# Performance work log

Measured on AMD Instinct MI355X. Metric: run time of the kernel, lower is better.

The kernel has to match this reference:

```python
import jax, jax.numpy as jnp
import numpy as np


def _gcn_conv(x, W, b, src, dst, n_nodes):
    """PyG-style GCNConv: XW, symmetric deg^-1/2 normalization over edges
    (with self-loops already included in src/dst), scatter-add to targets, + bias."""
    xw = x @ W  # [N, F_out]
    ones = jnp.ones(src.shape[0], dtype=xw.dtype)
    deg = jax.ops.segment_sum(ones, dst, num_segments=n_nodes)  # in-degree incl. self-loops
    dinv = jnp.where(deg > 0, jax.lax.rsqrt(jnp.maximum(deg, 1.0)), 0.0)
    norm = dinv[src] * dinv[dst]                        # [E]
    msgs = xw[src] * norm[:, None]                      # [E, F_out] gather + scale
    out = jax.ops.segment_sum(msgs, dst, num_segments=n_nodes)  # scatter-add
    return out + b


def setup_inputs() -> dict:
    key = jax.random.key(0)
    k1, k2, k3, k4 = jax.random.split(key, 4)
    N, E = 100000, 1600000
    IN, HID, OUT = 128, 64, 64
    x = jax.random.normal(k1, (N, IN), dtype=jnp.float32)
    edge_index = jax.random.randint(k2, (2, E), 0, N, dtype=jnp.int64)
    W1 = jax.random.normal(k3, (IN, HID), dtype=jnp.float32) * (1.0 / np.sqrt(IN))
    b1 = jnp.zeros((HID,), dtype=jnp.float32)
    W2 = jax.random.normal(k4, (HID, OUT), dtype=jnp.float32) * (1.0 / np.sqrt(HID))
    b2 = jnp.zeros((OUT,), dtype=jnp.float32)
    return {"x": x, "edge_index": edge_index, "W1": W1, "b1": b1, "W2": W2, "b2": b2}


def reference(x, edge_index, W1, b1, W2, b2):
    n_nodes = x.shape[0]
    # add self-loops (PyG GCNConv default add_self_loops=True)
    loops = jnp.arange(n_nodes, dtype=edge_index.dtype)
    src = jnp.concatenate([edge_index[0], loops])
    dst = jnp.concatenate([edge_index[1], loops])
    h = _gcn_conv(x, W1, b1, src, dst, n_nodes)
    h = jax.nn.relu(h)
    z = _gcn_conv(h, W2, b2, src, dst, n_nodes)
    return z
```

## Files before the change

### kernel.cpp

```cpp
#include <hip/hip_runtime.h>

#define IN_F 128
#define HID_F 64
#define BKT_SHIFT 9
#define BKT_SIZE 512
#define CHUNK 4096

typedef unsigned short ushort_t;
typedef __attribute__((ext_vector_type(8))) short bf16x8;
typedef __attribute__((ext_vector_type(4))) float f32x4;

__device__ inline ushort_t f2bf(float f) {
    unsigned u = __float_as_uint(f);
    u += 0x7FFFu + ((u >> 16) & 1u);
    return (ushort_t)(u >> 16);
}
__device__ inline float bf2f(ushort_t u) {
    return __uint_as_float((unsigned)u << 16);
}


__global__ __launch_bounds__(256) void k_bcount(const int* __restrict__ dst,
        int* __restrict__ gcount, int E) {
    __shared__ int hist[256];
    int tid = threadIdx.x;
    hist[tid] = 0;
    __syncthreads();
    int e0 = blockIdx.x * CHUNK, e1 = min(e0 + CHUNK, E);
    for (int e = e0 + tid; e < e1; e += 256)
        atomicAdd(&hist[dst[e] >> BKT_SHIFT], 1);
    __syncthreads();
    if (hist[tid]) atomicAdd(&gcount[tid], hist[tid]);
}

__global__ __launch_bounds__(256) void k_bscan(const int* __restrict__ gcount,
        int* __restrict__ bbase, int* __restrict__ gcursor,
        int* __restrict__ rowptr, int N, int E) {
    __shared__ int s[256];
    int tid = threadIdx.x;
    int c = gcount[tid];
    s[tid] = c;
    __syncthreads();
    for (int off = 1; off < 256; off <<= 1) {
        int v = (tid >= off) ? s[tid - off] : 0;
        __syncthreads();
        s[tid] += v;
        __syncthreads();
    }
    int excl = s[tid] - c;
    bbase[tid] = excl;
    gcursor[tid] = excl;
    if (tid == 255) bbase[256] = s[255];
    if (tid == 0) rowptr[N] = E;
}

__global__ __launch_bounds__(256) void k_bin(const int* __restrict__ src,
        const int* __restrict__ dst, int* __restrict__ gcursor,
        unsigned* __restrict__ gbin, int E) {
    __shared__ int hist[256];
    __shared__ int cur[256];
    int tid = threadIdx.x;
    hist[tid] = 0;
    __syncthreads();
    int e0 = blockIdx.x * CHUNK, e1 = min(e0 + CHUNK, E);
    for (int e = e0 + tid; e < e1; e += 256)
        atomicAdd(&hist[dst[e] >> BKT_SHIFT], 1);
    __syncthreads();
    if (hist[tid]) cur[tid] = atomicAdd(&gcursor[tid], hist[tid]);
    __syncthreads();
    for (int e = e0 + tid; e < e1; e += 256) {
        int d = dst[e];
        int b = d >> BKT_SHIFT;
        int p = atomicAdd(&cur[b], 1);
        gbin[p] = ((unsigned)(d & (BKT_SIZE - 1)) << 23) | (unsigned)src[e];
    }
}

__global__ __launch_bounds__(256) void k_fill2(const unsigned* __restrict__ gbin,
        const int* __restrict__ bbase, int* __restrict__ rowptr,
        float* __restrict__ dinv, int* __restrict__ col, int N) {
    __shared__ int cnt[BKT_SIZE];
    __shared__ int pos[BKT_SIZE];
    __shared__ int s[256];
    int tid = threadIdx.x;
    int b = blockIdx.x;
    int e0 = bbase[b], e1 = bbase[b + 1];
    cnt[tid] = 0; cnt[tid + 256] = 0;
    __syncthreads();
    for (int e = e0 + tid; e < e1; e += 256)
        atomicAdd(&cnt[gbin[e] >> 23], 1);
    __syncthreads();
    int c0 = cnt[2 * tid], c1 = cnt[2 * tid + 1];
    int p2 = c0 + c1;
    s[tid] = p2;
    __syncthreads();
    for (int off = 1; off < 256; off <<= 1) {
        int v = (tid >= off) ? s[tid - off] : 0;
        __syncthreads();
        s[tid] += v;
        __syncthreads();
    }
    int excl = s[tid] - p2;
    pos[2 * tid] = excl;
    pos[2 * tid + 1] = excl + c0;
    __syncthreads();
    int n0 = b << BKT_SHIFT;
    #pragma unroll
    for (int i = tid; i < BKT_SIZE; i += 256) {
        int n = n0 + i;
        if (n < N) {
            rowptr[n] = e0 + pos[i];
            dinv[n] = rsqrtf((float)cnt[i] + 1.0f);
        }
    }
    __syncthreads();
    for (int e = e0 + tid; e < e1; e += 256) {
        unsigned v = gbin[e];
        int p = atomicAdd(&pos[v >> 23], 1);
        col[e0 + p] = (int)(v & 0x7FFFFFu);
    }
}

__global__ void k_pack(const float* __restrict__ W1, const float* __restrict__ W2,
                       ushort_t* __restrict__ Bp1, ushort_t* __restrict__ Bp2) {
    int tid = blockIdx.x * 256 + threadIdx.x;
    int id = (tid < 8192) ? tid : tid - 8192;
    int j = id & 7, lane = (id >> 3) & 63, t = (id >> 9) & 3, s = id >> 11;
    int k = s * 32 + ((lane >> 4) << 3) + j;
    int n = t * 16 + (lane & 15);
    if (tid < 8192)        Bp1[id] = f2bf(W1[k * 64 + n]);
    else if (tid < 12288)  Bp2[id] = f2bf(W2[k * 64 + n]);
}

template<int K, typename AT>
__global__ __launch_bounds__(256) void k_gemm_mfma(const AT* __restrict__ A,
        const ushort_t* __restrict__ Bp, const float* __restrict__ dinv,
        ushort_t* __restrict__ out, int N) {
    int wave = threadIdx.x >> 6, lane = threadIdx.x & 63;
    int m = lane & 15, q = lane >> 4;
    int row0 = blockIdx.x * 64 + wave * 16;
    int arow = row0 + m;
    int arowc = (arow < N) ? arow : (N - 1);
    f32x4 acc[4] = {};
    #pragma unroll
    for (int s = 0; s < K / 32; ++s) {
        bf16x8 af;
        if constexpr (sizeof(AT) == 4) {
            const float* ap = (const float*)A + (size_t)arowc * K + s * 32 + q * 8;
            float4 x0 = *(const float4*)ap;
            float4 x1 = *(const float4*)(ap + 4);
            af[0] = (short)f2bf(x0.x); af[1] = (short)f2bf(x0.y);
            af[2] = (short)f2bf(x0.z); af[3] = (short)f2bf(x0.w);
            af[4] = (short)f2bf(x1.x); af[5] = (short)f2bf(x1.y);
            af[6] = (short)f2bf(x1.z); af[7] = (short)f2bf(x1.w);
        } else {
            af = *(const bf16x8*)((const ushort_t*)A + (size_t)arowc * K + s * 32 + q * 8);
        }
        #pragma unroll
        for (int t = 0; t < 4; ++t) {
            bf16x8 bf = *(const bf16x8*)(Bp + (size_t)((s * 4 + t) * 64 + lane) * 8);
            acc[t] = __builtin_amdgcn_mfma_f32_16x16x32_bf16(af, bf, acc[t], 0, 0, 0);
        }
    }
    int orow0 = row0 + q * 4;
    float4 d4 = *(const float4*)(dinv + orow0);
    #pragma unroll
    for (int r = 0; r < 4; ++r) {
        int row = orow0 + r;
        if (row < N) {
            float dn = (r == 0) ? d4.x : (r == 1) ? d4.y : (r == 2) ? d4.z : d4.w;
            #pragma unroll
            for (int t = 0; t < 4; ++t)
                out[(size_t)row * 64 + t * 16 + m] = f2bf(acc[t][r] * dn);
        }
    }
}

__global__ __launch_bounds__(256) void k_aggregate(const ushort_t* __restrict__ xws,
        const int* __restrict__ rowptr, const int* __restrict__ col,
        const float* __restrict__ dinv, const float* __restrict__ bias,
        float* __restrict__ outf, ushort_t* __restrict__ outb, int N, int relu_bf16) {
    int n = (blockIdx.x * 256 + threadIdx.x) >> 4;
    int i = threadIdx.x & 15;
    if (n >= N) return;
    int beg = rowptr[n], end = rowptr[n + 1];
    float dn = dinv[n];
    const ushort_t* base = xws + i * 4;
    ushort4 sv = *(const ushort4*)(base + (size_t)n * 64);
    float ac[4][4] = {};
    ac[0][0] = bf2f(sv.x); ac[0][1] = bf2f(sv.y);
    ac[0][2] = bf2f(sv.z); ac[0][3] = bf2f(sv.w);
    int e = beg;
    for (; e + 4 <= end; e += 4) {
        int c0 = col[e + 0], c1 = col[e + 1], c2 = col[e + 2], c3 = col[e + 3];
        ushort4 v0 = *(const ushort4*)(base + (size_t)c0 * 64);
        ushort4 v1 = *(const ushort4*)(base + (size_t)c1 * 64);
        ushort4 v2 = *(const ushort4*)(base + (size_t)c2 * 64);
        ushort4 v3 = *(const ushort4*)(base + (size_t)c3 * 64);
        ac[0][0] += bf2f(v0.x); ac[0][1] += bf2f(v0.y); ac[0][2] += bf2f(v0.z); ac[0][3] += bf2f(v0.w);
        ac[1][0] += bf2f(v1.x); ac[1][1] += bf2f(v1.y); ac[1][2] += bf2f(v1.z); ac[1][3] += bf2f(v1.w);
        ac[2][0] += bf2f(v2.x); ac[2][1] += bf2f(v2.y); ac[2][2] += bf2f(v2.z); ac[2][3] += bf2f(v2.w);
        ac[3][0] += bf2f(v3.x); ac[3][1] += bf2f(v3.y); ac[3][2] += bf2f(v3.z); ac[3][3] += bf2f(v3.w);
    }
    for (; e < end; ++e) {
        int c = col[e];
        ushort4 v = *(const ushort4*)(base + (size_t)c * 64);
        ac[0][0] += bf2f(v.x); ac[0][1] += bf2f(v.y);
        ac[0][2] += bf2f(v.z); ac[0][3] += bf2f(v.w);
    }
    float4 b4 = *(const float4*)(bias + i * 4);
    float r0 = dn * (ac[0][0] + ac[1][0] + ac[2][0] + ac[3][0]) + b4.x;
    float r1 = dn * (ac[0][1] + ac[1][1] + ac[2][1] + ac[3][1]) + b4.y;
    float r2 = dn * (ac[0][2] + ac[1][2] + ac[2][2] + ac[3][2]) + b4.z;
    float r3 = dn * (ac[0][3] + ac[1][3] + ac[2][3] + ac[3][3]) + b4.w;
    if (relu_bf16) {
        ushort4 o;
        o.x = f2bf(fmaxf(r0, 0.f)); o.y = f2bf(fmaxf(r1, 0.f));
        o.z = f2bf(fmaxf(r2, 0.f)); o.w = f2bf(fmaxf(r3, 0.f));
        *(ushort4*)(outb + (size_t)n * 64 + i * 4) = o;
    } else {
        float4 o = {r0, r1, r2, r3};
        *(float4*)(outf + (size_t)n * 64 + i * 4) = o;
    }
}


extern "C" void kernel_launch(void* const* d_in, const int* in_sizes, int n_in,
                              void* d_out, int out_size, void* d_ws, size_t ws_size,
                              hipStream_t stream) {
    const float* x  = (const float*)d_in[0];
    const int*   ei = (const int*)d_in[1];
    const float* W1 = (const float*)d_in[2];
    const float* b1 = (const float*)d_in[3];
    const float* W2 = (const float*)d_in[4];
    const float* b2 = (const float*)d_in[5];
    float* out = (float*)d_out;

    const int N = in_sizes[0] / IN_F;
    const int E = in_sizes[1] / 2;
    const int* src = ei;
    const int* dst = ei + E;

    char* ws = (char*)d_ws;
    const size_t MB = 1u << 20;
    int*      gcount  = (int*)     (ws + 0 * MB);
    int*      bbase   = (int*)     (ws + 4096);
    int*      gcursor = (int*)     (ws + 8192);
    ushort_t* Bp1     = (ushort_t*)(ws + 16384);
    ushort_t* Bp2     = (ushort_t*)(ws + 49152);
    int*      rowptr  = (int*)     (ws + 1 * MB);
    float*    dinv    = (float*)   (ws + 2 * MB);
    unsigned* gbin    = (unsigned*)(ws + 3 * MB);
    int*      col     = (int*)     (ws + 10 * MB);
    ushort_t* xws     = (ushort_t*)(ws + 20 * MB);
    ushort_t* h       = (ushort_t*)(ws + 36 * MB);

    const int nbE = (E + CHUNK - 1) / CHUNK;
    const int nbB = (N + BKT_SIZE - 1) / BKT_SIZE;
    const int nbG = (N + 63) / 64;
    const int nbA = (N * 16 + 255) / 256;

    hipMemsetAsync(gcount, 0, 256 * sizeof(int), stream);
    k_pack  <<<48, 256, 0, stream>>>(W1, W2, Bp1, Bp2);
    k_bcount<<<nbE, 256, 0, stream>>>(dst, gcount, E);
    k_bscan <<<1, 256, 0, stream>>>(gcount, bbase, gcursor, rowptr, N, E);
    k_bin   <<<nbE, 256, 0, stream>>>(src, dst, gcursor, gbin, E);
    k_fill2 <<<nbB, 256, 0, stream>>>(gbin, bbase, rowptr, dinv, col, N);

    k_gemm_mfma<IN_F, float>   <<<nbG, 256, 0, stream>>>(x, Bp1, dinv, xws, N);
    k_aggregate<<<nbA, 256, 0, stream>>>(xws, rowptr, col, dinv, b1, nullptr, h, N, 1);

    k_gemm_mfma<HID_F, ushort_t><<<nbG, 256, 0, stream>>>(h, Bp2, dinv, xws, N);
    k_aggregate<<<nbA, 256, 0, stream>>>(xws, rowptr, col, dinv, b2, out, nullptr, N, 0);
}
```

Measured before the change: 254.7 us.

## Use per-block histograms for binning and widen aggregate gathers to 16 bytes

The bucket-sort preprocessing now stores a histogram per block and scans it once in a single block. The scatter pass then reads precomputed offsets instead of rebuilding its local histogram and doing global atomics, and the memset is gone. Separately, the aggregation kernel uses 8 threads per node, each loading 8 bf16 values (16 bytes) per neighbor row, with an 8-way unrolled edge loop for more memory-level parallelism. The single-block serial scan over about 391 histogram rows adds latency, and 8 lanes per node doubles the per-thread register footprint.

```diff
diff --git a/kernel.cpp b/kernel.cpp
--- a/kernel.cpp
+++ b/kernel.cpp
@@ -8,6 +8,7 @@
 
 typedef unsigned short ushort_t;
 typedef __attribute__((ext_vector_type(8))) short bf16x8;
+typedef __attribute__((ext_vector_type(8))) unsigned short u16x8;
 typedef __attribute__((ext_vector_type(4))) float f32x4;
 
 __device__ inline ushort_t f2bf(float f) {
@@ -20,8 +21,8 @@
 }
 
 
-__global__ __launch_bounds__(256) void k_bcount(const int* __restrict__ dst,
-        int* __restrict__ gcount, int E) {
+__global__ __launch_bounds__(256) void k_hist(const int* __restrict__ dst,
+        int* __restrict__ ghist, int E) {
     __shared__ int hist[256];
     int tid = threadIdx.x;
     hist[tid] = 0;
@@ -30,44 +31,43 @@
     for (int e = e0 + tid; e < e1; e += 256)
         atomicAdd(&hist[dst[e] >> BKT_SHIFT], 1);
     __syncthreads();
-    if (hist[tid]) atomicAdd(&gcount[tid], hist[tid]);
-}
-
-__global__ __launch_bounds__(256) void k_bscan(const int* __restrict__ gcount,
-        int* __restrict__ bbase, int* __restrict__ gcursor,
-        int* __restrict__ rowptr, int N, int E) {
+    ghist[blockIdx.x * 256 + tid] = hist[tid];
+}
+
+__global__ __launch_bounds__(256) void k_scanhist(int* __restrict__ ghist,
+        int* __restrict__ gbase, int* __restrict__ bbase, int* __restrict__ rowptr,
+        int nb, int N, int E) {
     __shared__ int s[256];
-    int tid = threadIdx.x;
-    int c = gcount[tid];
-    s[tid] = c;
+    int t = threadIdx.x;
+    int run = 0;
+    for (int j = 0; j < nb; ++j) {
+        int v = ghist[j * 256 + t];
+        ghist[j * 256 + t] = run;
+        run += v;
+    }
+    s[t] = run;
     __syncthreads();
     for (int off = 1; off < 256; off <<= 1) {
-        int v = (tid >= off) ? s[tid - off] : 0;
-        __syncthreads();
-        s[tid] += v;
-        __syncthreads();
-    }
-    int excl = s[tid] - c;
-    bbase[tid] = excl;
-    gcursor[tid] = excl;
-    if (tid == 255) bbase[256] = s[255];
-    if (tid == 0) rowptr[N] = E;
-}
-
-__global__ __launch_bounds__(256) void k_bin(const int* __restrict__ src,
-        const int* __restrict__ dst, int* __restrict__ gcursor,
-        unsigned* __restrict__ gbin, int E) {
-    __shared__ int hist[256];
+        int v = (t >= off) ? s[t - off] : 0;
+        __syncthreads();
+        s[t] += v;
+        __syncthreads();
+    }
+    int base = s[t] - run;
+    gbase[t] = base;
+    bbase[t] = base;
+    if (t == 255) bbase[256] = s[255];
+    if (t == 0) rowptr[N] = E;
+}
+
+__global__ __launch_bounds__(256) void k_scatter(const int* __restrict__ src,
+        const int* __restrict__ dst, const int* __restrict__ ghist,
+        const int* __restrict__ gbase, unsigned* __restrict__ gbin, int E) {
     __shared__ int cur[256];
     int tid = threadIdx.x;
-    hist[tid] = 0;
+    cur[tid] = ghist[blockIdx.x * 256 + tid] + gbase[tid];
     __syncthreads();
     int e0 = blockIdx.x * CHUNK, e1 = min(e0 + CHUNK, E);
-    for (int e = e0 + tid; e < e1; e += 256)
-        atomicAdd(&hist[dst[e] >> BKT_SHIFT], 1);
-    __syncthreads();
-    if (hist[tid]) cur[tid] = atomicAdd(&gcursor[tid], hist[tid]);
-    __syncthreads();
     for (int e = e0 + tid; e < e1; e += 256) {
         int d = dst[e];
         int b = d >> BKT_SHIFT;
@@ -180,47 +180,64 @@
         const int* __restrict__ rowptr, const int* __restrict__ col,
         const float* __restrict__ dinv, const float* __restrict__ bias,
         float* __restrict__ outf, ushort_t* __restrict__ outb, int N, int relu_bf16) {
-    int n = (blockIdx.x * 256 + threadIdx.x) >> 4;
-    int i = threadIdx.x & 15;
+    int n = (blockIdx.x * 256 + threadIdx.x) >> 3;
+    int i = threadIdx.x & 7;
     if (n >= N) return;
     int beg = rowptr[n], end = rowptr[n + 1];
     float dn = dinv[n];
-    const ushort_t* base = xws + i * 4;
-    ushort4 sv = *(const ushort4*)(base + (size_t)n * 64);
-    float ac[4][4] = {};
-    ac[0][0] = bf2f(sv.x); ac[0][1] = bf2f(sv.y);
-    ac[0][2] = bf2f(sv.z); ac[0][3] = bf2f(sv.w);
+    const ushort_t* base = xws + i * 8;
+    u16x8 sv = *(const u16x8*)(base + (size_t)n * 64);
+    float a[8];
+    #pragma unroll
+    for (int k = 0; k < 8; ++k) a[k] = bf2f(sv[k]);
     int e = beg;
-    for (; e + 4 <= end; e += 4) {
-        int c0 = col[e + 0], c1 = col[e + 1], c2 = col[e + 2], c3 = col[e + 3];
-        ushort4 v0 = *(const ushort4*)(base + (size_t)c0 * 64);
-        ushort4 v1 = *(const ushort4*)(base + (size_t)c1 * 64);
-        ushort4 v2 = *(const ushort4*)(base + (size_t)c2 * 64);
-        ushort4 v3 = *(const ushort4*)(base + (size_t)c3 * 64);
-        ac[0][0] += bf2f(v0.x); ac[0][1] += bf2f(v0.y); ac[0][2] += bf2f(v0.z); ac[0][3] += bf2f(v0.w);
-        ac[1][0] += bf2f(v1.x); ac[1][1] += bf2f(v1.y); ac[1][2] += bf2f(v1.z); ac[1][3] += bf2f(v1.w);
-        ac[2][0] += bf2f(v2.x); ac[2][1] += bf2f(v2.y); ac[2][2] += bf2f(v2.z); ac[2][3] += bf2f(v2.w);
-        ac[3][0] += bf2f(v3.x); ac[3][1] += bf2f(v3.y); ac[3][2] += bf2f(v3.z); ac[3][3] += bf2f(v3.w);
+    for (; e + 8 <= end; e += 8) {
+        int c[8];
+        #pragma unroll
+        for (int j = 0; j < 8; ++j) c[j] = col[e + j];
+        u16x8 v[8];
+        #pragma unroll
+        for (int j = 0; j < 8; ++j) v[j] = *(const u16x8*)(base + (size_t)c[j] * 64);
+        #pragma unroll
+        for (int j = 0; j < 8; ++j)
+            #pragma unroll
+            for (int k = 0; k < 8; ++k) a[k] += bf2f(v[j][k]);
+    }
+    if (e + 4 <= end) {
+        int c[4];
+        #pragma unroll
+        for (int j = 0; j < 4; ++j) c[j] = col[e + j];
+        u16x8 v[4];
+        #pragma unroll
+        for (int j = 0; j < 4; ++j) v[j] = *(const u16x8*)(base + (size_t)c[j] * 64);
+        #pragma unroll
+        for (int j = 0; j < 4; ++j)
+            #pragma unroll
+            for (int k = 0; k < 8; ++k) a[k] += bf2f(v[j][k]);
+        e += 4;
     }
     for (; e < end; ++e) {
-        int c = col[e];
-        ushort4 v = *(const ushort4*)(base + (size_t)c * 64);
-        ac[0][0] += bf2f(v.x); ac[0][1] += bf2f(v.y);
-        ac[0][2] += bf2f(v.z); ac[0][3] += bf2f(v.w);
-    }
-    float4 b4 = *(const float4*)(bias + i * 4);
-    float r0 = dn * (ac[0][0] + ac[1][0] + ac[2][0] + ac[3][0]) + b4.x;
-    float r1 = dn * (ac[0][1] + ac[1][1] + ac[2][1] + ac[3][1]) + b4.y;
-    float r2 = dn * (ac[0][2] + ac[1][2] + ac[2][2] + ac[3][2]) + b4.z;
-    float r3 = dn * (ac[0][3] + ac[1][3] + ac[2][3] + ac[3][3]) + b4.w;
+        u16x8 v = *(const u16x8*)(base + (size_t)col[e] * 64);
+        #pragma unroll
+        for (int k = 0; k < 8; ++k) a[k] += bf2f(v[k]);
+    }
+    float4 b0 = *(const float4*)(bias + i * 8);
+    float4 b1 = *(const float4*)(bias + i * 8 + 4);
+    float r[8];
+    r[0] = dn * a[0] + b0.x; r[1] = dn * a[1] + b0.y;
+    r[2] = dn * a[2] + b0.z; r[3] = dn * a[3] + b0.w;
+    r[4] = dn * a[4] + b1.x; r[5] = dn * a[5] + b1.y;
+    r[6] = dn * a[6] + b1.z; r[7] = dn * a[7] + b1.w;
     if (relu_bf16) {
-        ushort4 o;
-        o.x = f2bf(fmaxf(r0, 0.f)); o.y = f2bf(fmaxf(r1, 0.f));
-        o.z = f2bf(fmaxf(r2, 0.f)); o.w = f2bf(fmaxf(r3, 0.f));
-        *(ushort4*)(outb + (size_t)n * 64 + i * 4) = o;
+        u16x8 o;
+        #pragma unroll
+        for (int k = 0; k < 8; ++k) o[k] = f2bf(fmaxf(r[k], 0.f));
+        *(u16x8*)(outb + (size_t)n * 64 + i * 8) = o;
     } else {
-        float4 o = {r0, r1, r2, r3};
-        *(float4*)(outf + (size_t)n * 64 + i * 4) = o;
+        float4 o0 = {r[0], r[1], r[2], r[3]};
+        float4 o1 = {r[4], r[5], r[6], r[7]};
+        *(float4*)(outf + (size_t)n * 64 + i * 8) = o0;
+        *(float4*)(outf + (size_t)n * 64 + i * 8 + 4) = o1;
     }
 }
 
@@ -243,29 +260,28 @@
 
     char* ws = (char*)d_ws;
     const size_t MB = 1u << 20;
-    int*      gcount  = (int*)     (ws + 0 * MB);
     int*      bbase   = (int*)     (ws + 4096);
-    int*      gcursor = (int*)     (ws + 8192);
+    int*      gbase   = (int*)     (ws + 8192);
     ushort_t* Bp1     = (ushort_t*)(ws + 16384);
     ushort_t* Bp2     = (ushort_t*)(ws + 49152);
     int*      rowptr  = (int*)     (ws + 1 * MB);
     float*    dinv    = (float*)   (ws + 2 * MB);
     unsigned* gbin    = (unsigned*)(ws + 3 * MB);
-    int*      col     = (int*)     (ws + 10 * MB);
+    int*      ghist   = (int*)     (ws + 10 * MB);
+    int*      col     = (int*)     (ws + 11 * MB);
     ushort_t* xws     = (ushort_t*)(ws + 20 * MB);
     ushort_t* h       = (ushort_t*)(ws + 36 * MB);
 
     const int nbE = (E + CHUNK - 1) / CHUNK;
     const int nbB = (N + BKT_SIZE - 1) / BKT_SIZE;
     const int nbG = (N + 63) / 64;
-    const int nbA = (N * 16 + 255) / 256;
-
-    hipMemsetAsync(gcount, 0, 256 * sizeof(int), stream);
-    k_pack  <<<48, 256, 0, stream>>>(W1, W2, Bp1, Bp2);
-    k_bcount<<<nbE, 256, 0, stream>>>(dst, gcount, E);
-    k_bscan <<<1, 256, 0, stream>>>(gcount, bbase, gcursor, rowptr, N, E);
-    k_bin   <<<nbE, 256, 0, stream>>>(src, dst, gcursor, gbin, E);
-    k_fill2 <<<nbB, 256, 0, stream>>>(gbin, bbase, rowptr, dinv, col, N);
+    const int nbA = (N * 8 + 255) / 256;
+
+    k_pack    <<<48, 256, 0, stream>>>(W1, W2, Bp1, Bp2);
+    k_hist    <<<nbE, 256, 0, stream>>>(dst, ghist, E);
+    k_scanhist<<<1, 256, 0, stream>>>(ghist, gbase, bbase, rowptr, nbE, N, E);
+    k_scatter <<<nbE, 256, 0, stream>>>(src, dst, ghist, gbase, gbin, E);
+    k_fill2   <<<nbB, 256, 0, stream>>>(gbin, bbase, rowptr, dinv, col, N);
 
     k_gemm_mfma<IN_F, float>   <<<nbG, 256, 0, stream>>>(x, Bp1, dinv, xws, N);
     k_aggregate<<<nbA, 256, 0, stream>>>(xws, rowptr, col, dinv, b1, nullptr, h, N, 1);
```

New measurement: 324.5 us. 1.27x slower.
